# Performance work log

Measured on AMD Instinct MI355X. Metric: run time of the kernel, lower is better.

## Reference

```python
import jax, jax.numpy as jnp
import numpy as np

OUTPUT_SIZE = (7, 7)
SPATIAL_SCALE = 0.25
SAMPLING_RATIO = 2


def setup_inputs() -> dict:
    key = jax.random.key(0)
    k1, k2, k3, k4, k5 = jax.random.split(key, 5)
    N, C, H, W = 2, 256, 200, 304
    R = 1000
    features = jax.random.normal(k1, (N, C, H, W), dtype=jnp.float32)
    # Boxes in IMAGE coordinates (image ~ 800x1216 since spatial_scale=0.25)
    img_h, img_w = H / SPATIAL_SCALE, W / SPATIAL_SCALE
    batch_idx = jax.random.randint(k2, (R,), 0, N).astype(jnp.float32)
    x1 = jax.random.uniform(k3, (R,), minval=0.0, maxval=img_w * 0.8)
    y1 = jax.random.uniform(k4, (R,), minval=0.0, maxval=img_h * 0.8)
    wh = jax.random.uniform(k5, (R, 2), minval=16.0, maxval=256.0)
    x2 = jnp.minimum(x1 + wh[:, 0], img_w - 1.0)
    y2 = jnp.minimum(y1 + wh[:, 1], img_h - 1.0)
    boxes = jnp.stack([batch_idx, x1, y1, x2, y2], axis=1).astype(jnp.float32)
    return {"features": features, "boxes": boxes}


def _axis_interp(coord, size):
    """torchvision bilinear_interpolate clamping along one axis.
    coord: float sample positions. Returns (low_idx, high_idx, frac, valid)."""
    valid = (coord >= -1.0) & (coord <= size)
    c = jnp.maximum(coord, 0.0)
    low_raw = jnp.floor(c).astype(jnp.int32)
    at_edge = low_raw >= size - 1
    low = jnp.where(at_edge, size - 1, low_raw)
    high = jnp.where(at_edge, size - 1, low_raw + 1)
    frac = jnp.where(at_edge, 0.0, c - low_raw.astype(c.dtype))
    return low, high, frac, valid


def roi_align(features, boxes, output_size, spatial_scale, sampling_ratio):
    N, C, H, W = features.shape
    PH, PW = output_size
    G = sampling_ratio
    b = boxes[:, 0].astype(jnp.int32)                      # [R]
    x1 = boxes[:, 1] * spatial_scale
    y1 = boxes[:, 2] * spatial_scale
    x2 = boxes[:, 3] * spatial_scale
    y2 = boxes[:, 4] * spatial_scale
    roi_w = jnp.maximum(x2 - x1, 1.0)
    roi_h = jnp.maximum(y2 - y1, 1.0)
    bin_h = roi_h / PH
    bin_w = roi_w / PW
    off = (jnp.arange(G, dtype=jnp.float32) + 0.5) / G     # [G] sample offsets in bin
    # per-axis sample coords: ys [R,PH,G], xs [R,PW,G]
    ys = y1[:, None, None] + (jnp.arange(PH, dtype=jnp.float32)[None, :, None] + off[None, None, :]) * bin_h[:, None, None]
    xs = x1[:, None, None] + (jnp.arange(PW, dtype=jnp.float32)[None, :, None] + off[None, None, :]) * bin_w[:, None, None]
    yl, yh, fy, vy = _axis_interp(ys, H)
    xl, xh, fx, vx = _axis_interp(xs, W)
    feat = features.transpose(0, 2, 3, 1)                  # [N,H,W,C]
    bb = b[:, None, None, None, None]                      # broadcast to [R,PH,G,PW,G]
    Y = lambda idx: idx[:, :, :, None, None]
    X = lambda idx: idx[:, None, None, :, :]
    # four corner gathers -> [R,PH,G,PW,G,C]
    v_ll = feat[bb, Y(yl), X(xl)]
    v_lh = feat[bb, Y(yl), X(xh)]
    v_hl = feat[bb, Y(yh), X(xl)]
    v_hh = feat[bb, Y(yh), X(xh)]
    fy_b = fy[:, :, :, None, None, None]
    fx_b = fx[:, None, None, :, :, None]
    interp = ((1 - fy_b) * (1 - fx_b) * v_ll + (1 - fy_b) * fx_b * v_lh
              + fy_b * (1 - fx_b) * v_hl + fy_b * fx_b * v_hh)
    valid = (vy[:, :, :, None, None] & vx[:, None, None, :, :])[..., None]
    interp = jnp.where(valid, interp, 0.0)
    pooled = interp.mean(axis=(2, 4))                      # avg over G*G samples -> [R,PH,PW,C]
    return pooled.transpose(0, 3, 1, 2)                    # [R,C,PH,PW]


def reference(features, boxes):
    return roi_align(features, boxes, OUTPUT_SIZE, SPATIAL_SCALE, SAMPLING_RATIO)
```

## Files before the change

### kernel.cpp

```cpp
#include <hip/hip_runtime.h>
#include <hip/hip_bf16.h>


constexpr int N_B  = 2;
constexpr int C_CH = 256;
constexpr int H_F  = 200;
constexpr int W_F  = 304;
constexpr int HW   = H_F * W_F;
constexpr int PH   = 7;
constexpr int PW   = 7;
constexpr int CELLS = PH * PW;
constexpr int CSTRIDE = 56;
constexpr float SCALE = 0.25f;

typedef float  v4f __attribute__((ext_vector_type(4)));

static __device__ __forceinline__ unsigned short f2bf(float f) {
    __hip_bfloat16 h = __float2bfloat16(f);
    return *reinterpret_cast<unsigned short*>(&h);
}
static __device__ __forceinline__ float blo(unsigned int u) {
    return __uint_as_float(u << 16);
}
static __device__ __forceinline__ float bhi(unsigned int u) {
    return __uint_as_float(u & 0xffff0000u);
}

__global__ __launch_bounds__(256) void transpose_nchw_nhwc_bf16(
    const float* __restrict__ in, unsigned short* __restrict__ out)
{
    __shared__ float tile[64][65];
    int tx = blockIdx.x * 64;
    int ty = blockIdx.y * 64;
    int n  = blockIdx.z;
    const float* ip = in  + (size_t)n * C_CH * HW;
    unsigned short* op = out + (size_t)n * HW * C_CH;

    int w4 = threadIdx.x & 15;
    int cr = threadIdx.x >> 4;
#pragma unroll
    for (int p = 0; p < 4; ++p) {
        int c = p * 16 + cr;
        v4f v = __builtin_nontemporal_load(
            (const v4f*)&ip[(size_t)(ty + c) * HW + tx + 4 * w4]);
        tile[c][4 * w4 + 0] = v.x;
        tile[c][4 * w4 + 1] = v.y;
        tile[c][4 * w4 + 2] = v.z;
        tile[c][4 * w4 + 3] = v.w;
    }
    __syncthreads();
    int cq = threadIdx.x & 15;
    int hr = threadIdx.x >> 4;
#pragma unroll
    for (int p = 0; p < 4; ++p) {
        int hw = p * 16 + hr;
        ushort4 v;
        v.x = f2bf(tile[4 * cq + 0][hw]);
        v.y = f2bf(tile[4 * cq + 1][hw]);
        v.z = f2bf(tile[4 * cq + 2][hw]);
        v.w = f2bf(tile[4 * cq + 3][hw]);
        *(ushort4*)&op[(size_t)(tx + hw) * C_CH + ty + 4 * cq] = v;
    }
}

static __device__ __forceinline__ void acc8(
    float* acc, uint4 ll, uint4 lh, uint4 hl, uint4 hh,
    float fxx, float fyy, float w)
{
#define ACC_PAIR(C, I0, I1)                                                   \
    { float a = blo(ll.C), b = blo(lh.C), c = blo(hl.C), d = blo(hh.C);       \
      float lo = a + fxx * (b - a), hi = c + fxx * (d - c);                   \
      acc[I0] += w * (lo + fyy * (hi - lo)); }                                \
    { float a = bhi(ll.C), b = bhi(lh.C), c = bhi(hl.C), d = bhi(hh.C);       \
      float lo = a + fxx * (b - a), hi = c + fxx * (d - c);                   \
      acc[I1] += w * (lo + fyy * (hi - lo)); }
    ACC_PAIR(x, 0, 1)
    ACC_PAIR(y, 2, 3)
    ACC_PAIR(z, 4, 5)
    ACC_PAIR(w, 6, 7)
#undef ACC_PAIR
}

__global__ __launch_bounds__(512) void roi_gather_nhwc(
    const unsigned short* __restrict__ feat_nhwc,
    const float* __restrict__ boxes,
    float* __restrict__ out, int R)
{
    __shared__ alignas(16) float lds[C_CH * CSTRIDE];
    int r = blockIdx.x;
    if (r >= R) return;
    int tid = threadIdx.x;
    int grp = tid >> 5;
    int ln  = tid & 31;
    int swz = ln & 7;

    const float* box = boxes + r * 5;
    int   b  = (int)box[0];
    float x1 = box[1] * SCALE;
    float y1 = box[2] * SCALE;
    float x2 = box[3] * SCALE;
    float y2 = box[4] * SCALE;
    float bin_w = fmaxf(x2 - x1, 1.0f) * (1.0f / PW);
    float bin_h = fmaxf(y2 - y1, 1.0f) * (1.0f / PH);

    const unsigned short* fb = feat_nhwc + (size_t)b * HW * C_CH + 8 * ln;

    for (int cell = grp; cell < CELLS; cell += 16) {
        int ph = cell / PW;
        int pw = cell - ph * PW;

        int   yl[2], yh[2]; float fy[2], vy[2];
#pragma unroll
        for (int iy = 0; iy < 2; ++iy) {
            float y = y1 + ((float)ph + (iy ? 0.75f : 0.25f)) * bin_h;
            vy[iy] = (y >= -1.0f && y <= (float)H_F) ? 1.0f : 0.0f;
            float cy = fmaxf(y, 0.0f);
            int ylr = (int)floorf(cy);
            bool e = (ylr >= H_F - 1);
            yl[iy] = e ? H_F - 1 : ylr;
            yh[iy] = e ? H_F - 1 : ylr + 1;
            fy[iy] = e ? 0.0f : cy - (float)ylr;
        }
        int   xl[2], xh[2]; float fx[2], vx[2];
#pragma unroll
        for (int ix = 0; ix < 2; ++ix) {
            float x = x1 + ((float)pw + (ix ? 0.75f : 0.25f)) * bin_w;
            vx[ix] = (x >= -1.0f && x <= (float)W_F) ? 1.0f : 0.0f;
            float cx = fmaxf(x, 0.0f);
            int xlr = (int)floorf(cx);
            bool e = (xlr >= W_F - 1);
            xl[ix] = e ? W_F - 1 : xlr;
            xh[ix] = e ? W_F - 1 : xlr + 1;
            fx[ix] = e ? 0.0f : cx - (float)xlr;
        }

        float acc[8] = {0.f, 0.f, 0.f, 0.f, 0.f, 0.f, 0.f, 0.f};

#pragma unroll
        for (int iy = 0; iy < 2; ++iy) {
            const unsigned short* rl = fb + (size_t)(yl[iy] * W_F) * C_CH;
            const unsigned short* rh = fb + (size_t)(yh[iy] * W_F) * C_CH;
            uint4 l0 = *(const uint4*)(rl + (size_t)xl[0] * C_CH);
            uint4 l1 = *(const uint4*)(rl + (size_t)xh[0] * C_CH);
            uint4 l2 = *(const uint4*)(rl + (size_t)xl[1] * C_CH);
            uint4 l3 = *(const uint4*)(rl + (size_t)xh[1] * C_CH);
            uint4 h0 = *(const uint4*)(rh + (size_t)xl[0] * C_CH);
            uint4 h1 = *(const uint4*)(rh + (size_t)xh[0] * C_CH);
            uint4 h2 = *(const uint4*)(rh + (size_t)xl[1] * C_CH);
            uint4 h3 = *(const uint4*)(rh + (size_t)xh[1] * C_CH);
            acc8(acc, l0, l1, h0, h1, fx[0], fy[iy], vy[iy] * vx[0]);
            acc8(acc, l2, l3, h2, h3, fx[1], fy[iy], vy[iy] * vx[1]);
        }

        int cellx = cell ^ swz;
#pragma unroll
        for (int j = 0; j < 8; ++j)
            lds[(8 * ln + j) * CSTRIDE + cellx] = acc[j] * 0.25f;
    }
    __syncthreads();

    float4* dst = (float4*)(out + (size_t)r * (C_CH * CELLS));
    for (int q = tid; q < (C_CH * CELLS) / 4; q += 512) {
        int w0 = 4 * q;
        float4 v;
        {
            int c = w0 / 49, ce = w0 - 49 * c;
            v.x = lds[c * CSTRIDE + (ce ^ ((c >> 3) & 7))];
        }
        {
            int wv = w0 + 1; int c = wv / 49, ce = wv - 49 * c;
            v.y = lds[c * CSTRIDE + (ce ^ ((c >> 3) & 7))];
        }
        {
            int wv = w0 + 2; int c = wv / 49, ce = wv - 49 * c;
            v.z = lds[c * CSTRIDE + (ce ^ ((c >> 3) & 7))];
        }
        {
            int wv = w0 + 3; int c = wv / 49, ce = wv - 49 * c;
            v.w = lds[c * CSTRIDE + (ce ^ ((c >> 3) & 7))];
        }
        dst[q] = v;
    }
}

__global__ __launch_bounds__(256) void roi_align_fallback(
    const float* __restrict__ feat,
    const float* __restrict__ boxes,
    float* __restrict__ out, int total)
{
    int idx = blockIdx.x * 256 + threadIdx.x;
    if (idx >= total) return;
    int pw = idx % PW;
    int t  = idx / PW;
    int ph = t % PH;
    t /= PH;
    int c = t & (C_CH - 1);
    int r = t >> 8;

    const float* box = boxes + r * 5;
    int   b  = (int)box[0];
    float x1 = box[1] * SCALE;
    float y1 = box[2] * SCALE;
    float x2 = box[3] * SCALE;
    float y2 = box[4] * SCALE;
    float bin_w = fmaxf(x2 - x1, 1.0f) * (1.0f / PW);
    float bin_h = fmaxf(y2 - y1, 1.0f) * (1.0f / PH);
    const float* fp = feat + ((size_t)b * C_CH + c) * HW;

    float acc = 0.0f;
#pragma unroll
    for (int iy = 0; iy < 2; ++iy) {
        float y = y1 + ((float)ph + (iy ? 0.75f : 0.25f)) * bin_h;
        bool vy = (y >= -1.0f) && (y <= (float)H_F);
        float cy = fmaxf(y, 0.0f);
        int ylr = (int)floorf(cy);
        int yl, yh; float fyv;
        if (ylr >= H_F - 1) { yl = H_F - 1; yh = H_F - 1; fyv = 0.0f; }
        else                { yl = ylr;     yh = ylr + 1; fyv = cy - (float)ylr; }
#pragma unroll
        for (int ix = 0; ix < 2; ++ix) {
            float x = x1 + ((float)pw + (ix ? 0.75f : 0.25f)) * bin_w;
            bool vx = (x >= -1.0f) && (x <= (float)W_F);
            float cx = fmaxf(x, 0.0f);
            int xlr = (int)floorf(cx);
            int xlv, xhv; float fxv;
            if (xlr >= W_F - 1) { xlv = W_F - 1; xhv = W_F - 1; fxv = 0.0f; }
            else                { xlv = xlr;     xhv = xlr + 1; fxv = cx - (float)xlr; }
            if (vy && vx) {
                const float* rl = fp + yl * W_F;
                const float* rh = fp + yh * W_F;
                float vll = rl[xlv], vlh = rl[xhv], vhl = rh[xlv], vhh = rh[xhv];
                float vlo = vll + fxv * (vlh - vll);
                float vhi = vhl + fxv * (vhh - vhl);
                acc += vlo + fyv * (vhi - vlo);
            }
        }
    }
    out[idx] = acc * 0.25f;
}

extern "C" void kernel_launch(void* const* d_in, const int* in_sizes, int n_in,
                              void* d_out, int out_size, void* d_ws, size_t ws_size,
                              hipStream_t stream) {
    const float* feat  = (const float*)d_in[0];
    const float* boxes = (const float*)d_in[1];
    float* out = (float*)d_out;
    int R = in_sizes[1] / 5;

    size_t need = (size_t)N_B * C_CH * HW * sizeof(unsigned short);
    if (ws_size >= need) {
        unsigned short* nhwc = (unsigned short*)d_ws;
        dim3 tg(HW / 64, C_CH / 64, N_B);
        transpose_nchw_nhwc_bf16<<<tg, 256, 0, stream>>>(feat, nhwc);
        roi_gather_nhwc<<<R, 512, 0, stream>>>(nhwc, boxes, out, R);
    } else {
        int total = out_size;
        roi_align_fallback<<<(total + 255) / 256, 256, 0, stream>>>(feat, boxes, out, total);
    }
}
```

Measured before the change: 235.4 us.

## Sort ROIs spatially and remap blocks per XCD for L2 locality

Adds a single-block bitonic sort kernel that orders ROIs by batch index and a serpentine stripe key over box centers, producing a permutation. The gather kernel reads ROIs through this permutation and remaps block IDs so that consecutive sorted ROIs land on the same XCD, so each XCD's L2 serves spatially nearby boxes and overlapping feature reads are reused. The cost is an extra kernel launch and a serialized sort. Output indexing must still use the original ROI id.

```diff
diff --git a/kernel.cpp b/kernel.cpp
--- a/kernel.cpp
+++ b/kernel.cpp
@@ -11,6 +11,7 @@
 constexpr int PW   = 7;
 constexpr int CELLS = PH * PW;
 constexpr int CSTRIDE = 56;
+constexpr int NXCD = 8;
 constexpr float SCALE = 0.25f;
 
 typedef float  v4f __attribute__((ext_vector_type(4)));
@@ -24,6 +25,47 @@
 }
 static __device__ __forceinline__ float bhi(unsigned int u) {
     return __uint_as_float(u & 0xffff0000u);
+}
+
+__global__ __launch_bounds__(1024) void sort_rois(
+    const float* __restrict__ boxes, unsigned int* __restrict__ perm, int R)
+{
+    int t = threadIdx.x;
+    if (R > 1024) {
+        for (int i = t; i < R; i += 1024) perm[i] = (unsigned int)i;
+        return;
+    }
+    __shared__ unsigned int k[1024];
+    unsigned int key = 0xFFFFFFFFu;
+    if (t < R) {
+        const float* box = boxes + t * 5;
+        int b  = (int)box[0];
+        float yc = (box[2] + box[4]) * 0.5f * SCALE;
+        float xc = (box[1] + box[3]) * 0.5f * SCALE;
+        int yq = min(max((int)yc, 0), H_F - 1);
+        int xq = min(max((int)xc, 0), W_F - 1);
+        int stripe = yq >> 4;
+        int xs = (stripe & 1) ? (W_F - 1 - xq) : xq;
+        unsigned int s = ((unsigned int)b << 13) | ((unsigned int)stripe << 9)
+                       | (unsigned int)xs;
+        key = (s << 10) | (unsigned int)t;
+    }
+    k[t] = key;
+    __syncthreads();
+#pragma unroll 1
+    for (int size = 2; size <= 1024; size <<= 1) {
+#pragma unroll 1
+        for (int stride = size >> 1; stride > 0; stride >>= 1) {
+            int j = t ^ stride;
+            if (j > t) {
+                unsigned int a = k[t], c = k[j];
+                bool up = ((t & size) == 0);
+                if ((a > c) == up) { k[t] = c; k[j] = a; }
+            }
+            __syncthreads();
+        }
+    }
+    if (t < R) perm[t] = k[t] & 1023u;
 }
 
 __global__ __launch_bounds__(256) void transpose_nchw_nhwc_bf16(
@@ -84,11 +126,19 @@
 __global__ __launch_bounds__(512) void roi_gather_nhwc(
     const unsigned short* __restrict__ feat_nhwc,
     const float* __restrict__ boxes,
+    const unsigned int* __restrict__ perm,
     float* __restrict__ out, int R)
 {
     __shared__ alignas(16) float lds[C_CH * CSTRIDE];
-    int r = blockIdx.x;
+    int pos = blockIdx.x;
+    if (pos >= R) return;
+    if ((R & (NXCD - 1)) == 0) {
+        int cpx = R / NXCD;
+        pos = (pos & (NXCD - 1)) * cpx + (pos >> 3);
+    }
+    int r = (int)perm[pos];
     if (r >= R) return;
+
     int tid = threadIdx.x;
     int grp = tid >> 5;
     int ln  = tid & 31;
@@ -247,12 +297,16 @@
     float* out = (float*)d_out;
     int R = in_sizes[1] / 5;
 
-    size_t need = (size_t)N_B * C_CH * HW * sizeof(unsigned short);
+    size_t need_nhwc = (size_t)N_B * C_CH * HW * sizeof(unsigned short);
+    size_t perm_off  = (need_nhwc + 255) & ~(size_t)255;
+    size_t need      = perm_off + (size_t)((R > 1024 ? R : 1024)) * sizeof(unsigned int);
     if (ws_size >= need) {
         unsigned short* nhwc = (unsigned short*)d_ws;
+        unsigned int*   perm = (unsigned int*)((char*)d_ws + perm_off);
+        sort_rois<<<1, 1024, 0, stream>>>(boxes, perm, R);
         dim3 tg(HW / 64, C_CH / 64, N_B);
         transpose_nchw_nhwc_bf16<<<tg, 256, 0, stream>>>(feat, nhwc);
-        roi_gather_nhwc<<<R, 512, 0, stream>>>(nhwc, boxes, out, R);
+        roi_gather_nhwc<<<R, 512, 0, stream>>>(nhwc, boxes, perm, out, R);
     } else {
         int total = out_size;
         roi_align_fallback<<<(total + 255) / 256, 256, 0, stream>>>(feat, boxes, out, total);
```

After: 230.3 us, median of 2. 1.02x faster.
